# Optimization experiments

Measured on AMD Instinct MI355X. Metric: run time of the kernel, lower is better.

Reference implementation:

```python
import jax, jax.numpy as jnp
import numpy as np

N, E, F, H, EA = 50000, 500000, 2000, 128, 2
NUM_BOND_TYPES = 100
COORDS_RANGE = 10.0
NORM_FACTOR = 100.0


def setup_inputs() -> dict:
    key = jax.random.key(0)
    ks = jax.random.split(key, 20)

    def lin(k, i, o, gain=1.0):
        # xavier-uniform-ish init, stored as [in, out] so forward is x @ W + b
        lim = gain * np.sqrt(6.0 / (i + o))
        return jax.random.uniform(k, (i, o), jnp.float32, -lim, lim)

    inp = {
        "h_a": jax.random.normal(ks[0], (N, H), jnp.float32),
        "x_a": jax.random.normal(ks[1], (N, 3), jnp.float32),
        "e_a_idx": jax.random.randint(ks[2], (2, E), 0, N),
        "e_a_type": jax.random.randint(ks[3], (E,), 0, NUM_BOND_TYPES),
        "e_a_attr": jax.random.normal(ks[4], (E, EA), jnp.float32),
        "coord_diff_a": jax.random.normal(ks[5], (E, 3), jnp.float32),
        "h_f": jax.random.normal(ks[6], (F, H), jnp.float32),
        "x_f": jax.random.normal(ks[7], (F, 3), jnp.float32),
        "bm_mat": jax.random.normal(ks[8], (N, F), jnp.float32) / np.sqrt(F),
        # parameters
        "bond_emb": jax.random.normal(ks[9], (NUM_BOND_TYPES, H), jnp.float32),
        "aW1": lin(ks[10], 2 * H + EA + H, H), "ab1": jnp.zeros((H,), jnp.float32),
        "aW2": lin(ks[11], H, H), "ab2": jnp.zeros((H,), jnp.float32),
        "aW3": lin(ks[12], H, 1, gain=0.001),  # xavier gain=0.001, no bias
        "fW1": lin(ks[13], 2 * H + EA, H), "fb1": jnp.zeros((H,), jnp.float32),
        "fW2": lin(ks[14], H, H), "fb2": jnp.zeros((H,), jnp.float32),
        "fW3": lin(ks[15], H, 1, gain=0.001),
    }
    return inp


def reference(h_a, x_a, e_a_idx, e_a_type, e_a_attr, coord_diff_a, h_f, x_f, bm_mat,
              bond_emb, aW1, ab1, aW2, ab2, aW3, fW1, fb1, fW2, fb2, fW3):
    silu = jax.nn.silu
    row, col = e_a_idx[0], e_a_idx[1]

    be = bond_emb[e_a_type]                              # [E, H]
    coord_diff_f = x_a - bm_mat @ x_f                    # [N, 3]
    radial_f = jnp.sum(coord_diff_f ** 2, axis=1, keepdims=True)  # [N, 1]
    norm_f = jnp.sqrt(radial_f + 1e-8)
    coord_diff_f = coord_diff_f / (norm_f + 1.0)

    inp_atom = jnp.concatenate([h_a[row], h_a[col], e_a_attr, be], axis=1)        # [E, 3H+2]
    inp_frag = jnp.concatenate([h_a, bm_mat @ h_f, radial_f, radial_f], axis=1)   # [N, 2H+2]

    m_atom = silu(silu(inp_atom @ aW1 + ab1) @ aW2 + ab2) @ aW3  # [E, 1]
    m_frag = silu(silu(inp_frag @ fW1 + fb1) @ fW2 + fb2) @ fW3  # [N, 1]

    trans_atom = coord_diff_a * jnp.tanh(m_atom) * COORDS_RANGE  # [E, 3]
    trans_frag = coord_diff_f * jnp.tanh(m_frag) * COORDS_RANGE  # [N, 3]

    agg_atom = jax.ops.segment_sum(trans_atom, row, num_segments=x_a.shape[0]) / NORM_FACTOR
    return x_a + agg_atom + trans_frag
```

## Files before the change

### kernel.cpp

```cpp
#include <hip/hip_runtime.h>
#include <hip/hip_bf16.h>


typedef __attribute__((ext_vector_type(8))) short bfrag8;
typedef __attribute__((ext_vector_type(16))) float f32x16;
typedef __attribute__((ext_vector_type(4))) float f32x4v;

#define MFMA32(A, B, C) __builtin_amdgcn_mfma_f32_32x32x16_bf16((A), (B), (C), 0, 0, 0)

__device__ __forceinline__ f32x16 zero16() {
  f32x16 v;
#pragma unroll
  for (int i = 0; i < 16; ++i) v[i] = 0.0f;
  return v;
}

__device__ __forceinline__ unsigned short bf16bits(float x) {
  __hip_bfloat16 b = __float2bfloat16(x);
  unsigned short u;
  __builtin_memcpy(&u, &b, 2);
  return u;
}

__device__ __forceinline__ unsigned pk2(float lo, float hi) {
  return (unsigned)bf16bits(lo) | ((unsigned)bf16bits(hi) << 16);
}

__device__ __forceinline__ bfrag8 ldfrag(const unsigned short* p) {
  return *reinterpret_cast<const bfrag8*>(p);
}

__device__ __forceinline__ bfrag8 frag4(unsigned f0, unsigned f1, unsigned f2, unsigned f3) {
  union { unsigned u[4]; bfrag8 v; } q;
  q.u[0] = f0; q.u[1] = f1; q.u[2] = f2; q.u[3] = f3;
  return q.v;
}

__device__ __forceinline__ float silu_f(float x) { return x / (1.0f + __expf(-x)); }

__global__ __launch_bounds__(256) void prep_kernel(
    const float* __restrict__ h_a, const float* __restrict__ bond,
    const float* __restrict__ h_f,
    const float* __restrict__ aW1, const float* __restrict__ ab1,
    const float* __restrict__ aW2,
    const float* __restrict__ fW1, const float* __restrict__ fW2,
    unsigned short* __restrict__ h_bf, unsigned short* __restrict__ bond_bf,
    float* __restrict__ hfp,
    unsigned short* __restrict__ W1aT, unsigned short* __restrict__ W1bT,
    unsigned short* __restrict__ W1cT, unsigned short* __restrict__ W1eT,
    unsigned short* __restrict__ W2T,
    unsigned short* __restrict__ fW1aT, unsigned short* __restrict__ fW2T,
    float* __restrict__ agg,
    int N, int NB, int F) {
  const int t = threadIdx.x;
  int bid = blockIdx.x;
  const int G_A = (N * 16 + 255) >> 8;
  const int G_B = (NB * 16 + 255) >> 8;
  const int G_H = (F + 1) >> 1;

  if (bid < G_A + G_B) {
    const float* src = (bid < G_A) ? h_a : bond;
    unsigned short* dst = (bid < G_A) ? h_bf : bond_bf;
    int rows = (bid < G_A) ? N : NB;
    int idx = (bid < G_A ? bid : bid - G_A) * 256 + t;
    if (idx < rows * 16) {
      int row = idx >> 4, g = idx & 15;
      int h = g & 1, kc = g >> 1;
      const f32x4v* s = reinterpret_cast<const f32x4v*>(src + (size_t)row * 128 + g * 8);
      f32x4v v0 = s[0], v1 = s[1];
      unsigned* d = reinterpret_cast<unsigned*>(dst + (size_t)row * 128 + h * 64 + kc * 8);
      d[0] = pk2(v0[0], v0[1]);
      d[1] = pk2(v0[2], v0[3]);
      d[2] = pk2(v1[0], v1[1]);
      d[3] = pk2(v1[2], v1[3]);
    }
    return;
  }
  bid -= G_A + G_B;
  if (bid < G_H) {
    int f = bid * 2 + (t >> 7), n = t & 127;
    if (f < F) {
      float acc = 0.0f;
#pragma unroll 8
      for (int k = 0; k < 128; ++k)
        acc += h_f[(size_t)f * 128 + k] * fW1[(size_t)(128 + k) * 128 + n];
      hfp[(size_t)f * 128 + n] = acc;
    }
    return;
  }
  bid -= G_H;
  if (bid < 6 * 64) {
    int p = bid >> 6;
    int tt = (bid & 63) * 256 + t;
    int j = tt & 7, l = (tt >> 3) & 63, rem = tt >> 9;
    int nt = rem & 3, kc = rem >> 2;
    int k = kc * 16 + ((l >> 5) << 3) + j;
    int n = nt * 32 + (l & 31);
    const float* W;
    unsigned short* D;
    switch (p) {
      case 0: W = aW1;             D = W1aT;  break;
      case 1: W = aW1 + 128 * 128; D = W1bT;  break;
      case 2: W = aW1 + 258 * 128; D = W1cT;  break;
      case 3: W = aW2;             D = W2T;   break;
      case 4: W = fW1;             D = fW1aT; break;
      default: W = fW2;            D = fW2T;  break;
    }
    D[tt] = bf16bits(W[(size_t)k * 128 + n]);
    return;
  }
  bid -= 6 * 64;
  if (bid < 8) {
    int tt = bid * 256 + t;
    if (tt < 4 * 64 * 8) {
      int j = tt & 7, l = (tt >> 3) & 63, nt = (tt >> 9) & 3;
      int k = ((l >> 5) << 3) + j;
      int n = nt * 32 + (l & 31);
      float v = (k == 0) ? aW1[(size_t)256 * 128 + n]
              : (k == 1) ? aW1[(size_t)257 * 128 + n]
              : (k == 2) ? ab1[n] : 0.0f;
      W1eT[tt] = bf16bits(v);
    }
    return;
  }
  bid -= 8;
  {
    int i4 = (bid * 256 + t) * 4;
    if (i4 + 3 < N * 3) {
      *reinterpret_cast<f32x4v*>(agg + i4) = f32x4v{0.f, 0.f, 0.f, 0.f};
    } else {
      for (int c = 0; c < 4; ++c)
        if (i4 + c < N * 3) agg[i4 + c] = 0.0f;
    }
  }
}

__global__ void pack_bmat_kernel(const float* __restrict__ hfp, const float* __restrict__ x_f,
                                 unsigned short* __restrict__ dst, int total) {
  int t = blockIdx.x * blockDim.x + threadIdx.x;
  if (t >= total) return;
  int j = t & 7, l = (t >> 3) & 63, rem = t >> 9;
  int nt = rem % 5, kc = rem / 5;
  int k = kc * 16 + ((l >> 5) << 3) + j;
  int n = nt * 32 + (l & 31);
  float v;
  if (n < 128) v = hfp[(size_t)k * 128 + n];
  else if (n < 131) v = x_f[(size_t)k * 3 + (n - 128)];
  else v = 0.0f;
  dst[t] = bf16bits(v);
}

__global__ __launch_bounds__(256, 2) void fused_k1_k3(
    const float* __restrict__ bm, const unsigned short* __restrict__ bmT,
    float* __restrict__ k1T,
    const unsigned short* __restrict__ h_bf, const unsigned short* __restrict__ bond_bf,
    const int* __restrict__ eidx, const int* __restrict__ etype,
    const float* __restrict__ eattr, const float* __restrict__ cda,
    const unsigned short* __restrict__ W1aT, const unsigned short* __restrict__ W1bT,
    const unsigned short* __restrict__ W1cT, const unsigned short* __restrict__ W1eT,
    const unsigned short* __restrict__ W2T,
    const float* __restrict__ ab2, const float* __restrict__ aW3,
    float* __restrict__ agg,
    int N, int F, int E, int G1) {
  const int lane = threadIdx.x & 63;
  const int wid = threadIdx.x >> 6;
  const int h = lane >> 5;
  const int ln = lane & 31;

  if ((int)blockIdx.x < G1) {
    const int m = blockIdx.x * 128 + wid * 32 + ln;
    const int mc = (m < N) ? m : (N - 1);
    const float* bp = bm + (size_t)mc * F + h * 8;
    const int KC = F >> 4;

    f32x16 acc[5];
#pragma unroll
    for (int i = 0; i < 5; ++i) acc[i] = zero16();

    f32x4v a0 = *reinterpret_cast<const f32x4v*>(bp);
    f32x4v a1 = *reinterpret_cast<const f32x4v*>(bp + 4);
    f32x4v b0 = *reinterpret_cast<const f32x4v*>(bp + 16);
    f32x4v b1 = *reinterpret_cast<const f32x4v*>(bp + 20);
    for (int kc = 0; kc < KC; ++kc) {
      f32x4v c0 = a0, c1 = a1;
      a0 = b0; a1 = b1;
      if (kc + 2 < KC) {
        b0 = *reinterpret_cast<const f32x4v*>(bp + (size_t)(kc + 2) * 16);
        b1 = *reinterpret_cast<const f32x4v*>(bp + (size_t)(kc + 2) * 16 + 4);
      }
      bfrag8 b = frag4(pk2(c0[0], c0[1]), pk2(c0[2], c0[3]), pk2(c1[0], c1[1]), pk2(c1[2], c1[3]));
      const unsigned short* wp = bmT + ((size_t)kc * 5 * 64 + lane) * 8;
#pragma unroll
      for (int nt = 0; nt < 5; ++nt) acc[nt] = MFMA32(ldfrag(wp + nt * 512), b, acc[nt]);
    }
    if (m < N) {
#pragma unroll
      for (int nt = 0; nt < 5; ++nt)
#pragma unroll
        for (int r = 0; r < 16; ++r) {
          int n = nt * 32 + (r & 3) + 8 * (r >> 2) + 4 * h;
          if (n < 131) k1T[(size_t)n * N + m] = acc[nt][r];
        }
    }
    return;
  }

  const int e = (blockIdx.x - G1) * 128 + wid * 32 + ln;
  const bool valid = (e < E);
  const int ec = valid ? e : (E - 1);
  const int row = eidx[ec];
  const int col = eidx[(size_t)E + ec];
  const int typ = etype[ec];
  const float e0 = eattr[2 * (size_t)ec];
  const float e1 = eattr[2 * (size_t)ec + 1];

  const unsigned short* hr = h_bf + (size_t)row * 128 + h * 64;
  const unsigned short* hc = h_bf + (size_t)col * 128 + h * 64;
  const unsigned short* bb = bond_bf + (size_t)typ * 128 + h * 64;

  f32x16 acc[4];
#pragma unroll
  for (int q = 0; q < 4; ++q) acc[q] = zero16();

#pragma unroll
  for (int kc = 0; kc < 8; ++kc) {
    bfrag8 b = ldfrag(hr + kc * 8);
    const unsigned short* wp = W1aT + ((size_t)(kc * 4) * 64 + lane) * 8;
#pragma unroll
    for (int nt = 0; nt < 4; ++nt) acc[nt] = MFMA32(ldfrag(wp + nt * 512), b, acc[nt]);
  }
#pragma unroll
  for (int kc = 0; kc < 8; ++kc) {
    bfrag8 b = ldfrag(hc + kc * 8);
    const unsigned short* wp = W1bT + ((size_t)(kc * 4) * 64 + lane) * 8;
#pragma unroll
    for (int nt = 0; nt < 4; ++nt) acc[nt] = MFMA32(ldfrag(wp + nt * 512), b, acc[nt]);
  }
#pragma unroll
  for (int kc = 0; kc < 8; ++kc) {
    bfrag8 b = ldfrag(bb + kc * 8);
    const unsigned short* wp = W1cT + ((size_t)(kc * 4) * 64 + lane) * 8;
#pragma unroll
    for (int nt = 0; nt < 4; ++nt) acc[nt] = MFMA32(ldfrag(wp + nt * 512), b, acc[nt]);
  }
  {
    unsigned u0 = h ? 0u : pk2(e0, e1);
    unsigned u1 = h ? 0u : 0x00003F80u;
    bfrag8 b = frag4(u0, u1, 0u, 0u);
    const unsigned short* wp = W1eT + (size_t)lane * 8;
#pragma unroll
    for (int nt = 0; nt < 4; ++nt) acc[nt] = MFMA32(ldfrag(wp + nt * 512), b, acc[nt]);
  }

  unsigned w[32];
#pragma unroll
  for (int nt = 0; nt < 4; ++nt)
#pragma unroll
    for (int p = 0; p < 8; ++p)
      w[nt * 8 + p] = pk2(silu_f(acc[nt][2 * p]), silu_f(acc[nt][2 * p + 1]));

#pragma unroll
  for (int q = 0; q < 4; ++q) acc[q] = zero16();
#pragma unroll
  for (int kc = 0; kc < 8; ++kc) {
    const int base = (kc >> 1) * 8 + (kc & 1) * 4;
    unsigned a0 = w[base + 0], a1 = w[base + 1], a2 = w[base + 2], a3 = w[base + 3];
    unsigned s0 = (unsigned)__shfl_xor((int)a0, 32);
    unsigned s1 = (unsigned)__shfl_xor((int)a1, 32);
    unsigned s2 = (unsigned)__shfl_xor((int)a2, 32);
    unsigned s3 = (unsigned)__shfl_xor((int)a3, 32);
    bfrag8 b = frag4(h ? s2 : a0, h ? s3 : a1, h ? a2 : s0, h ? a3 : s1);
    const unsigned short* wp = W2T + ((size_t)(kc * 4) * 64 + lane) * 8;
#pragma unroll
    for (int nt = 0; nt < 4; ++nt) acc[nt] = MFMA32(ldfrag(wp + nt * 512), b, acc[nt]);
  }

  float part = 0.0f;
#pragma unroll
  for (int nt = 0; nt < 4; ++nt)
#pragma unroll
    for (int r = 0; r < 16; ++r) {
      int n = nt * 32 + (r & 3) + 8 * (r >> 2) + 4 * h;
      part += silu_f(acc[nt][r] + ab2[n]) * aW3[n];
    }
  float mv = part + __shfl_xor(part, 32);

  if (valid) {
    float t = tanhf(mv) * 0.1f;
    if (h == 0) {
      atomicAdd(agg + 3 * (size_t)row + 0, cda[3 * (size_t)ec + 0] * t);
      atomicAdd(agg + 3 * (size_t)row + 1, cda[3 * (size_t)ec + 1] * t);
    } else {
      atomicAdd(agg + 3 * (size_t)row + 2, cda[3 * (size_t)ec + 2] * t);
    }
  }
}

__global__ __launch_bounds__(256) void k2_frag(
    const float* __restrict__ x_a, const unsigned short* __restrict__ h_bf,
    const float* __restrict__ k1T, const float* __restrict__ agg,
    const unsigned short* __restrict__ fW1aT, const unsigned short* __restrict__ fW2T,
    const float* __restrict__ fW1, const float* __restrict__ fb1,
    const float* __restrict__ fb2, const float* __restrict__ fW3,
    float* __restrict__ out, int N) {
  const int lane = threadIdx.x & 63;
  const int wid = threadIdx.x >> 6;
  const int h = lane >> 5;
  const int ln = lane & 31;
  const int i = blockIdx.x * 128 + wid * 32 + ln;
  const bool valid = (i < N);
  const int ic = valid ? i : (N - 1);

  float cd[3];
  float radial = 0.0f;
#pragma unroll
  for (int c = 0; c < 3; ++c) {
    float v = x_a[3 * (size_t)ic + c] - k1T[(size_t)(128 + c) * N + ic];
    cd[c] = v;
    radial += v * v;
  }

  f32x16 acc[4];
#pragma unroll
  for (int q = 0; q < 4; ++q) acc[q] = zero16();
  const unsigned short* hp = h_bf + (size_t)ic * 128 + h * 64;
#pragma unroll
  for (int kc = 0; kc < 8; ++kc) {
    bfrag8 b = ldfrag(hp + kc * 8);
    const unsigned short* wp = fW1aT + ((size_t)(kc * 4) * 64 + lane) * 8;
#pragma unroll
    for (int nt = 0; nt < 4; ++nt) acc[nt] = MFMA32(ldfrag(wp + nt * 512), b, acc[nt]);
  }

  unsigned w[32];
#pragma unroll
  for (int nt = 0; nt < 4; ++nt)
#pragma unroll
    for (int p = 0; p < 8; ++p) {
      const int r0 = 2 * p;
      const int n0 = nt * 32 + (r0 & 3) + 8 * (r0 >> 2) + 4 * h;
      const int n1 = n0 + 1;
      float q0 = acc[nt][r0] + k1T[(size_t)n0 * N + ic]
               + radial * (fW1[(size_t)256 * 128 + n0] + fW1[(size_t)257 * 128 + n0]) + fb1[n0];
      float q1 = acc[nt][r0 + 1] + k1T[(size_t)n1 * N + ic]
               + radial * (fW1[(size_t)256 * 128 + n1] + fW1[(size_t)257 * 128 + n1]) + fb1[n1];
      w[nt * 8 + p] = pk2(silu_f(q0), silu_f(q1));
    }

#pragma unroll
  for (int q = 0; q < 4; ++q) acc[q] = zero16();
#pragma unroll
  for (int kc = 0; kc < 8; ++kc) {
    const int base = (kc >> 1) * 8 + (kc & 1) * 4;
    unsigned a0 = w[base + 0], a1 = w[base + 1], a2 = w[base + 2], a3 = w[base + 3];
    unsigned s0 = (unsigned)__shfl_xor((int)a0, 32);
    unsigned s1 = (unsigned)__shfl_xor((int)a1, 32);
    unsigned s2 = (unsigned)__shfl_xor((int)a2, 32);
    unsigned s3 = (unsigned)__shfl_xor((int)a3, 32);
    bfrag8 b = frag4(h ? s2 : a0, h ? s3 : a1, h ? a2 : s0, h ? a3 : s1);
    const unsigned short* wp = fW2T + ((size_t)(kc * 4) * 64 + lane) * 8;
#pragma unroll
    for (int nt = 0; nt < 4; ++nt) acc[nt] = MFMA32(ldfrag(wp + nt * 512), b, acc[nt]);
  }

  float part = 0.0f;
#pragma unroll
  for (int nt = 0; nt < 4; ++nt)
#pragma unroll
    for (int r = 0; r < 16; ++r) {
      int n = nt * 32 + (r & 3) + 8 * (r >> 2) + 4 * h;
      part += silu_f(acc[nt][r] + fb2[n]) * fW3[n];
    }
  float mv = part + __shfl_xor(part, 32);

  if (valid && h == 0) {
    float nrm = sqrtf(radial + 1e-8f);
    float s = tanhf(mv) * 10.0f / (nrm + 1.0f);
#pragma unroll
    for (int c = 0; c < 3; ++c)
      out[3 * (size_t)i + c] = x_a[3 * (size_t)i + c] + cd[c] * s + agg[3 * (size_t)i + c];
  }
}


extern "C" void kernel_launch(void* const* d_in, const int* in_sizes, int n_in,
                              void* d_out, int out_size, void* d_ws, size_t ws_size,
                              hipStream_t stream) {
  const float* h_a    = (const float*)d_in[0];
  const float* x_a    = (const float*)d_in[1];
  const int*   e_idx  = (const int*)d_in[2];
  const int*   e_type = (const int*)d_in[3];
  const float* e_attr = (const float*)d_in[4];
  const float* cda    = (const float*)d_in[5];
  const float* h_f    = (const float*)d_in[6];
  const float* x_f    = (const float*)d_in[7];
  const float* bm     = (const float*)d_in[8];
  const float* bond   = (const float*)d_in[9];
  const float* aW1    = (const float*)d_in[10];
  const float* ab1    = (const float*)d_in[11];
  const float* aW2    = (const float*)d_in[12];
  const float* ab2    = (const float*)d_in[13];
  const float* aW3    = (const float*)d_in[14];
  const float* fW1    = (const float*)d_in[15];
  const float* fb1    = (const float*)d_in[16];
  const float* fW2    = (const float*)d_in[17];
  const float* fb2    = (const float*)d_in[18];
  const float* fW3    = (const float*)d_in[19];
  float* out = (float*)d_out;

  const int N  = in_sizes[0] / 128;
  const int E  = in_sizes[2] / 2;
  const int F  = in_sizes[6] / 128;
  const int NB = in_sizes[9] / 128;
  const int KC = F / 16;

  char* wsp = (char*)d_ws;
  size_t off = 0;
  auto alloc = [&](size_t bytes) -> char* {
    char* p = wsp + off;
    off += (bytes + 255) & ~(size_t)255;
    return p;
  };
  unsigned short* h_bf    = (unsigned short*)alloc((size_t)N * 128 * 2);
  unsigned short* bond_bf = (unsigned short*)alloc((size_t)NB * 128 * 2);
  float*          hfp     = (float*)alloc((size_t)F * 128 * 4);
  unsigned short* bmT     = (unsigned short*)alloc((size_t)KC * 5 * 64 * 8 * 2);
  unsigned short* W1aT    = (unsigned short*)alloc(8 * 4 * 64 * 8 * 2);
  unsigned short* W1bT    = (unsigned short*)alloc(8 * 4 * 64 * 8 * 2);
  unsigned short* W1cT    = (unsigned short*)alloc(8 * 4 * 64 * 8 * 2);
  unsigned short* W2T     = (unsigned short*)alloc(8 * 4 * 64 * 8 * 2);
  unsigned short* fW1aT   = (unsigned short*)alloc(8 * 4 * 64 * 8 * 2);
  unsigned short* fW2T    = (unsigned short*)alloc(8 * 4 * 64 * 8 * 2);
  unsigned short* W1eT    = (unsigned short*)alloc(1 * 4 * 64 * 8 * 2);
  float*          k1T     = (float*)alloc((size_t)131 * N * 4);
  float*          agg     = (float*)alloc((size_t)N * 3 * 4);

  const int G_A = (N * 16 + 255) >> 8;
  const int G_B = (NB * 16 + 255) >> 8;
  const int G_H = (F + 1) >> 1;
  const int G_P = 6 * 64;
  const int G_E2 = 8;
  const int G_Z = (N * 3 + 1023) >> 10;
  prep_kernel<<<G_A + G_B + G_H + G_P + G_E2 + G_Z, 256, 0, stream>>>(
      h_a, bond, h_f, aW1, ab1, aW2, fW1, fW2,
      h_bf, bond_bf, hfp, W1aT, W1bT, W1cT, W1eT, W2T, fW1aT, fW2T, agg,
      N, NB, F);

  {
    int total = KC * 5 * 64 * 8;
    pack_bmat_kernel<<<(total + 255) / 256, 256, 0, stream>>>(hfp, x_f, bmT, total);
  }

  const int G1 = (N + 127) / 128;
  const int G3 = (E + 127) / 128;
  fused_k1_k3<<<G1 + G3, 256, 0, stream>>>(
      bm, bmT, k1T,
      h_bf, bond_bf, e_idx, e_type, e_attr, cda,
      W1aT, W1bT, W1cT, W1eT, W2T, ab2, aW3, agg,
      N, F, E, G1);

  k2_frag<<<(N + 127) / 128, 256, 0, stream>>>(x_a, h_bf, k1T, agg, fW1aT, fW2T,
                                               fW1, fb1, fb2, fW3, out, N);
}
```

Before: 381.2 us.

## Split fused kernel and stage bm tiles through swizzled double-buffered LDS

Splits the fused GEMM/edge kernel back into two launches. The bm@[h_f|x_f] GEMM becomes a 512-thread kernel that loads coalesced 64-column tiles of bm into XOR-swizzled, double-buffered shared memory as bf16, prefetching the next tile into registers while MFMAs run. This targets the strided per-lane global reads of the 400 MB bm matrix in the old path. The cost is losing the overlap that came from co-scheduling the GEMM and edge blocks in one launch, plus an extra launch and a block barrier per tile.

```diff
diff --git a/kernel.cpp b/kernel.cpp
--- a/kernel.cpp
+++ b/kernel.cpp
@@ -150,9 +150,101 @@
   dst[t] = bf16bits(v);
 }
 
-__global__ __launch_bounds__(256, 2) void fused_k1_k3(
+__global__ __launch_bounds__(512, 1) void k1_gemm(
     const float* __restrict__ bm, const unsigned short* __restrict__ bmT,
-    float* __restrict__ k1T,
+    float* __restrict__ k1T, int N, int F) {
+  __shared__ __align__(16) char lds[2][256 * 128];
+  const int t = threadIdx.x;
+  const int lane = t & 63;
+  const int w = t >> 6;
+  const int h = lane >> 5;
+  const int ln = lane & 31;
+  const int m0 = blockIdx.x * 256;
+  const int NT = (F + 63) >> 6;
+
+  f32x16 acc[5];
+#pragma unroll
+  for (int i = 0; i < 5; ++i) acc[i] = zero16();
+
+  int srow[8], sch[8];
+  const float* sptr[8];
+#pragma unroll
+  for (int p = 0; p < 8; ++p) {
+    int c = p * 512 + t;
+    srow[p] = c >> 4;
+    sch[p] = c & 15;
+    int gr = m0 + srow[p];
+    if (gr >= N) gr = N - 1;
+    sptr[p] = bm + (size_t)gr * F;
+  }
+
+  const int myrow = w * 32 + ln;
+  const int rsw = (myrow & 7) << 4;
+
+  f32x4v sregs[8];
+#pragma unroll
+  for (int p = 0; p < 8; ++p) {
+    int gk = sch[p] * 4;
+    if (gk > F - 4) gk = F - 4;
+    sregs[p] = *reinterpret_cast<const f32x4v*>(sptr[p] + gk);
+  }
+#pragma unroll
+  for (int p = 0; p < 8; ++p) {
+    int byte = srow[p] * 128 + ((sch[p] * 8) ^ ((srow[p] & 7) << 4));
+    union { unsigned u[2]; unsigned long long ull; } q;
+    q.u[0] = pk2(sregs[p][0], sregs[p][1]);
+    q.u[1] = pk2(sregs[p][2], sregs[p][3]);
+    *reinterpret_cast<unsigned long long*>(&lds[0][byte]) = q.ull;
+  }
+  __syncthreads();
+
+  int cur = 0;
+  for (int kt = 0; kt < NT; ++kt) {
+    const bool more = (kt + 1 < NT);
+    if (more) {
+#pragma unroll
+      for (int p = 0; p < 8; ++p) {
+        int gk = (kt + 1) * 64 + sch[p] * 4;
+        if (gk > F - 4) gk = F - 4;
+        sregs[p] = *reinterpret_cast<const f32x4v*>(sptr[p] + gk);
+      }
+    }
+    const int kcCount = ((F - kt * 64) >> 4) < 4 ? ((F - kt * 64) >> 4) : 4;
+    for (int kc = 0; kc < kcCount; ++kc) {
+      bfrag8 b = *reinterpret_cast<const bfrag8*>(
+          &lds[cur][myrow * 128 + ((kc * 32 + h * 16) ^ rsw)]);
+      const int kcg = kt * 4 + kc;
+      const unsigned short* wp = bmT + ((size_t)kcg * 5 * 64 + lane) * 8;
+#pragma unroll
+      for (int nt = 0; nt < 5; ++nt) acc[nt] = MFMA32(ldfrag(wp + nt * 512), b, acc[nt]);
+    }
+    if (more) {
+#pragma unroll
+      for (int p = 0; p < 8; ++p) {
+        int byte = srow[p] * 128 + ((sch[p] * 8) ^ ((srow[p] & 7) << 4));
+        union { unsigned u[2]; unsigned long long ull; } q;
+        q.u[0] = pk2(sregs[p][0], sregs[p][1]);
+        q.u[1] = pk2(sregs[p][2], sregs[p][3]);
+        *reinterpret_cast<unsigned long long*>(&lds[cur ^ 1][byte]) = q.ull;
+      }
+    }
+    __syncthreads();
+    cur ^= 1;
+  }
+
+  const int m = m0 + myrow;
+  if (m < N) {
+#pragma unroll
+    for (int nt = 0; nt < 5; ++nt)
+#pragma unroll
+      for (int r = 0; r < 16; ++r) {
+        int n = nt * 32 + (r & 3) + 8 * (r >> 2) + 4 * h;
+        if (n < 131) k1T[(size_t)n * N + m] = acc[nt][r];
+      }
+  }
+}
+
+__global__ __launch_bounds__(256) void k3_atom(
     const unsigned short* __restrict__ h_bf, const unsigned short* __restrict__ bond_bf,
     const int* __restrict__ eidx, const int* __restrict__ etype,
     const float* __restrict__ eattr, const float* __restrict__ cda,
@@ -160,52 +252,12 @@
     const unsigned short* __restrict__ W1cT, const unsigned short* __restrict__ W1eT,
     const unsigned short* __restrict__ W2T,
     const float* __restrict__ ab2, const float* __restrict__ aW3,
-    float* __restrict__ agg,
-    int N, int F, int E, int G1) {
+    float* __restrict__ agg, int E) {
   const int lane = threadIdx.x & 63;
   const int wid = threadIdx.x >> 6;
   const int h = lane >> 5;
   const int ln = lane & 31;
-
-  if ((int)blockIdx.x < G1) {
-    const int m = blockIdx.x * 128 + wid * 32 + ln;
-    const int mc = (m < N) ? m : (N - 1);
-    const float* bp = bm + (size_t)mc * F + h * 8;
-    const int KC = F >> 4;
-
-    f32x16 acc[5];
-#pragma unroll
-    for (int i = 0; i < 5; ++i) acc[i] = zero16();
-
-    f32x4v a0 = *reinterpret_cast<const f32x4v*>(bp);
-    f32x4v a1 = *reinterpret_cast<const f32x4v*>(bp + 4);
-    f32x4v b0 = *reinterpret_cast<const f32x4v*>(bp + 16);
-    f32x4v b1 = *reinterpret_cast<const f32x4v*>(bp + 20);
-    for (int kc = 0; kc < KC; ++kc) {
-      f32x4v c0 = a0, c1 = a1;
-      a0 = b0; a1 = b1;
-      if (kc + 2 < KC) {
-        b0 = *reinterpret_cast<const f32x4v*>(bp + (size_t)(kc + 2) * 16);
-        b1 = *reinterpret_cast<const f32x4v*>(bp + (size_t)(kc + 2) * 16 + 4);
-      }
-      bfrag8 b = frag4(pk2(c0[0], c0[1]), pk2(c0[2], c0[3]), pk2(c1[0], c1[1]), pk2(c1[2], c1[3]));
-      const unsigned short* wp = bmT + ((size_t)kc * 5 * 64 + lane) * 8;
-#pragma unroll
-      for (int nt = 0; nt < 5; ++nt) acc[nt] = MFMA32(ldfrag(wp + nt * 512), b, acc[nt]);
-    }
-    if (m < N) {
-#pragma unroll
-      for (int nt = 0; nt < 5; ++nt)
-#pragma unroll
-        for (int r = 0; r < 16; ++r) {
-          int n = nt * 32 + (r & 3) + 8 * (r >> 2) + 4 * h;
-          if (n < 131) k1T[(size_t)n * N + m] = acc[nt][r];
-        }
-    }
-    return;
-  }
-
-  const int e = (blockIdx.x - G1) * 128 + wid * 32 + ln;
+  const int e = blockIdx.x * 128 + wid * 32 + ln;
   const bool valid = (e < E);
   const int ec = valid ? e : (E - 1);
   const int row = eidx[ec];
@@ -286,12 +338,12 @@
   float mv = part + __shfl_xor(part, 32);
 
   if (valid) {
-    float t = tanhf(mv) * 0.1f;
+    float tt = tanhf(mv) * 0.1f;
     if (h == 0) {
-      atomicAdd(agg + 3 * (size_t)row + 0, cda[3 * (size_t)ec + 0] * t);
-      atomicAdd(agg + 3 * (size_t)row + 1, cda[3 * (size_t)ec + 1] * t);
+      atomicAdd(agg + 3 * (size_t)row + 0, cda[3 * (size_t)ec + 0] * tt);
+      atomicAdd(agg + 3 * (size_t)row + 1, cda[3 * (size_t)ec + 1] * tt);
     } else {
-      atomicAdd(agg + 3 * (size_t)row + 2, cda[3 * (size_t)ec + 2] * t);
+      atomicAdd(agg + 3 * (size_t)row + 2, cda[3 * (size_t)ec + 2] * tt);
     }
   }
 }
@@ -451,13 +503,10 @@
     pack_bmat_kernel<<<(total + 255) / 256, 256, 0, stream>>>(hfp, x_f, bmT, total);
   }
 
-  const int G1 = (N + 127) / 128;
-  const int G3 = (E + 127) / 128;
-  fused_k1_k3<<<G1 + G3, 256, 0, stream>>>(
-      bm, bmT, k1T,
-      h_bf, bond_bf, e_idx, e_type, e_attr, cda,
-      W1aT, W1bT, W1cT, W1eT, W2T, ab2, aW3, agg,
-      N, F, E, G1);
+  k1_gemm<<<(N + 255) / 256, 512, 0, stream>>>(bm, bmT, k1T, N, F);
+
+  k3_atom<<<(E + 127) / 128, 256, 0, stream>>>(h_bf, bond_bf, e_idx, e_type, e_attr, cda,
+                                               W1aT, W1bT, W1cT, W1eT, W2T, ab2, aW3, agg, E);
 
   k2_frag<<<(N + 127) / 128, 256, 0, stream>>>(x_a, h_bf, k1T, agg, fW1aT, fW2T,
                                                fW1, fb1, fb2, fW3, out, N);
```

New measurement: 405.8 us. 6.4% more time.
